# Optimization experiments

Measured on AMD Instinct MI355X. Metric: run time of the kernel, lower is better.

The kernel has to match this reference:

```python
import jax, jax.numpy as jnp
import numpy as np
from jax import lax

C = 128
HEADS = 4
HEAD_DIM = C // HEADS
SCALE = HEAD_DIM ** (-0.5)


def conv2d(x, w, b, pad):
    # x: (B, Cin, H, W), w: (Cout, Cin, kh, kw)
    y = lax.conv_general_dilated(
        x, w, window_strides=(1, 1), padding=[(pad, pad), (pad, pad)],
        dimension_numbers=("NCHW", "OIHW", "NCHW"))
    return y + b[None, :, None, None]


def setup_inputs() -> dict:
    key = jax.random.key(0)
    ks = jax.random.split(key, 16)
    B, H, W = 2, 64, 64
    fan_1x1 = 1.0 / np.sqrt(C)
    fan_3x3a = 1.0 / np.sqrt(1 * 9)
    fan_3x3b = 1.0 / np.sqrt((C // 4) * 9)
    inp = {
        "sr_feat": jax.random.normal(ks[0], (B, C, H, W), jnp.float32),
        "seg_mask": jax.random.uniform(ks[1], (B, 1, H, W), jnp.float32),
        "Wq": jax.random.uniform(ks[2], (C, C, 1, 1), jnp.float32, -fan_1x1, fan_1x1),
        "bq": jnp.zeros((C,), jnp.float32),
        "Wm1": jax.random.uniform(ks[3], (C // 4, 1, 3, 3), jnp.float32, -fan_3x3a, fan_3x3a),
        "bm1": jnp.zeros((C // 4,), jnp.float32),
        "Wm2": jax.random.uniform(ks[4], (C, C // 4, 3, 3), jnp.float32, -fan_3x3b, fan_3x3b),
        "bm2": jnp.zeros((C,), jnp.float32),
        "Wk": jax.random.uniform(ks[5], (C, C, 1, 1), jnp.float32, -fan_1x1, fan_1x1),
        "bk": jnp.zeros((C,), jnp.float32),
        "Wv": jax.random.uniform(ks[6], (C, C, 1, 1), jnp.float32, -fan_1x1, fan_1x1),
        "bv": jnp.zeros((C,), jnp.float32),
        "Wo": jax.random.uniform(ks[7], (C, C, 1, 1), jnp.float32, -fan_1x1, fan_1x1),
        "bo": jnp.zeros((C,), jnp.float32),
    }
    return inp


def reference(sr_feat, seg_mask, Wq, bq, Wm1, bm1, Wm2, bm2, Wk, bk, Wv, bv, Wo, bo):
    B, Cc, H, W = sr_feat.shape
    # mask_embed: conv3x3 -> relu -> conv3x3 (seg_mask already at (H, W))
    mask_feat = conv2d(jax.nn.relu(conv2d(seg_mask, Wm1, bm1, 1)), Wm2, bm2, 1)
    q = conv2d(sr_feat, Wq, bq, 0)
    k = conv2d(mask_feat, Wk, bk, 0)
    v = conv2d(mask_feat, Wv, bv, 0)
    hw = H * W
    # (B, C, HW) -> (B, heads, HW, head_dim)
    def split_heads(t):
        return t.reshape(B, HEADS, HEAD_DIM, hw).transpose(0, 1, 3, 2)
    qh, kh, vh = split_heads(q), split_heads(k), split_heads(v)
    attn = jnp.einsum("bhqd,bhkd->bhqk", qh, kh) * SCALE
    attn = jax.nn.softmax(attn, axis=-1)
    guided = jnp.einsum("bhqk,bhkd->bhqd", attn, vh)  # (B, heads, HW, head_dim)
    guided = guided.transpose(0, 1, 3, 2).reshape(B, Cc, H, W)
    return conv2d(guided, Wo, bo, 0) + sr_feat
```

## Files before the change

kernel.cpp:

```cpp
#include <hip/hip_runtime.h>
#include <hip/hip_bf16.h>

#define HW 4096
#define CC 128
#define SCALE_LOG2E (0.17677669529663687f * 1.4426950408889634f)
#define KSPLIT 8
#define H1PAD 4096

typedef short bf16x8 __attribute__((ext_vector_type(8)));
typedef float f32x4 __attribute__((ext_vector_type(4)));

static __device__ __forceinline__ unsigned short f2bf(float f) {
  unsigned int u = __float_as_uint(f);
  unsigned int r = (u + 0x7fffu + ((u >> 16) & 1u)) >> 16;
  return (unsigned short)r;
}
static __device__ __forceinline__ unsigned int pk2bf(float lo, float hi) {
  return __builtin_amdgcn_perm(__float_as_uint(hi), __float_as_uint(lo),
                               0x07060302u);
}
static __device__ __forceinline__ unsigned int pk2bf_rne(float lo, float hi) {
  return (unsigned int)f2bf(lo) | ((unsigned int)f2bf(hi) << 16);
}
static __device__ __forceinline__ f32x4 mfma16(bf16x8 a, bf16x8 b, f32x4 c) {
  return __builtin_amdgcn_mfma_f32_16x16x32_bf16(a, b, c, 0, 0, 0);
}

__global__ __launch_bounds__(256) void wcast_kernel(
    const float* __restrict__ Wq, const float* __restrict__ Wk,
    const float* __restrict__ Wv, const float* __restrict__ Wo,
    unsigned short* __restrict__ wbf) {
  int i = blockIdx.x * 256 + threadIdx.x;
  int which = i >> 14, j = i & 16383;
  const float* src = which == 0 ? Wq : which == 1 ? Wk : which == 2 ? Wv : Wo;
  float v = src[j];
  if (which == 0) v *= SCALE_LOG2E;
  wbf[i] = f2bf(v);
}

__global__ __launch_bounds__(256) void wcast2_kernel(
    const float* __restrict__ Wm2, unsigned short* __restrict__ wm2t) {
  int i = blockIdx.x * 256 + threadIdx.x;
  int tap = i >> 12;
  int rem = i & 4095;
  int co = rem >> 5, ci = rem & 31;
  wm2t[i] = f2bf(Wm2[co * 288 + ci * 9 + tap]);
}

__global__ __launch_bounds__(256) void conv1_relu_kernel(
    const float* __restrict__ seg, const float* __restrict__ Wm1,
    const float* __restrict__ bm1, unsigned short* __restrict__ h1p) {
  __shared__ float wls[288];
  const int t = threadIdx.x;
  for (int j = t; j < 288; j += 256) wls[j] = Wm1[j];
  const int idx = blockIdx.x * 256 + t;
  const int b = idx >> 12, p = idx & 4095;
  const int x = p & 63, y = p >> 6;
  const float* sb = seg + b * HW;
  float pix[9];
#pragma unroll
  for (int tap = 0; tap < 9; ++tap) {
    int dy = tap / 3 - 1, dx = tap % 3 - 1;
    int xx = x + dx, yy = y + dy;
    bool valid = ((unsigned)xx < 64u) & ((unsigned)yy < 64u);
    pix[tap] = valid ? sb[yy * 64 + xx] : 0.f;
  }
  __syncthreads();
  unsigned int pk[16];
#pragma unroll
  for (int cg = 0; cg < 16; ++cg) {
    float s0 = bm1[2 * cg], s1 = bm1[2 * cg + 1];
#pragma unroll
    for (int tap = 0; tap < 9; ++tap) {
      s0 += wls[(2 * cg) * 9 + tap] * pix[tap];
      s1 += wls[(2 * cg + 1) * 9 + tap] * pix[tap];
    }
    pk[cg] = pk2bf_rne(fmaxf(s0, 0.f), fmaxf(s1, 0.f));
  }
  unsigned short* dst = h1p + (size_t)idx * 32;
#pragma unroll
  for (int g = 0; g < 4; ++g) *(uint4*)(dst + g * 8) = *(uint4*)&pk[g * 4];
}

__global__ __launch_bounds__(256) void conv2_mfma(
    const unsigned short* __restrict__ h1p, const unsigned short* __restrict__ wm2t,
    const float* __restrict__ bm2, unsigned short* __restrict__ mfT) {
  const int b   = blockIdx.y;
  const int px0 = blockIdx.x * 32;
  const int t   = threadIdx.x;
  const int w = t >> 6, lane = t & 63, col = lane & 15, quad = lane >> 4;

  bf16x8 afrag[9][2];
#pragma unroll
  for (int tap = 0; tap < 9; ++tap) {
    const unsigned short* wb =
        wm2t + ((size_t)tap * 128 + w * 32 + col) * 32 + quad * 8;
    afrag[tap][0] = *(const bf16x8*)wb;
    afrag[tap][1] = *(const bf16x8*)(wb + 16 * 32);
  }

  const unsigned short* xb = h1p + (size_t)b * HW * 32;
  f32x4 acc[2][2] = {};
  const bf16x8 zf = {0, 0, 0, 0, 0, 0, 0, 0};

  const int px[2] = {px0 + col, px0 + 16 + col};
  const int xx[2] = {px[0] & 63, px[1] & 63};
  const int yy[2] = {px[0] >> 6, px[1] >> 6};

#pragma unroll
  for (int tap = 0; tap < 9; ++tap) {
    const int dy = tap / 3 - 1, dx = tap % 3 - 1;
    const int shift = dy * 64 + dx;
#pragma unroll
    for (int pt = 0; pt < 2; ++pt) {
      bool valid = ((unsigned)(xx[pt] + dx) < 64u) & ((unsigned)(yy[pt] + dy) < 64u);
      bf16x8 bf = *(const bf16x8*)(xb + (size_t)(px[pt] + shift) * 32 + quad * 8);
      bf = valid ? bf : zf;
      acc[0][pt] = mfma16(afrag[tap][0], bf, acc[0][pt]);
      acc[1][pt] = mfma16(afrag[tap][1], bf, acc[1][pt]);
    }
  }

#pragma unroll
  for (int ct = 0; ct < 2; ++ct) {
    float4 bb = *(const float4*)(bm2 + w * 32 + ct * 16 + quad * 4);
#pragma unroll
    for (int pt = 0; pt < 2; ++pt) {
      int co = w * 32 + ct * 16 + quad * 4;
      uint2 pk = {pk2bf_rne(acc[ct][pt][0] + bb.x, acc[ct][pt][1] + bb.y),
                  pk2bf_rne(acc[ct][pt][2] + bb.z, acc[ct][pt][3] + bb.w)};
      *(uint2*)(mfT + ((size_t)b * HW + px[pt]) * CC + co) = pk;
    }
  }
}

__global__ __launch_bounds__(256) void conv_q_mfma(
    const float* __restrict__ in, const unsigned short* __restrict__ wq,
    const float* __restrict__ bq, unsigned short* __restrict__ qt) {
  const int b   = blockIdx.y;
  const int px0 = blockIdx.x * 32;
  const int t   = threadIdx.x;
  const int w = t >> 6, lane = t & 63, col = lane & 15, quad = lane >> 4;

  __shared__ unsigned short xT[32][136];
  for (int r = 0; r < 16; ++r) {
    int idx = r * 256 + t;
    int ci = idx >> 5, px = idx & 31;
    xT[px][ci] = f2bf(in[((size_t)b * CC + ci) * HW + px0 + px]);
  }
  __syncthreads();

  f32x4 acc[2][2] = {};
  const unsigned short* wbase = wq + (size_t)(w * 32 + col) * CC + quad * 8;
#pragma unroll
  for (int ks = 0; ks < 4; ++ks) {
    bf16x8 a0 = *(const bf16x8*)(wbase + ks * 32);
    bf16x8 a1 = *(const bf16x8*)(wbase + 16 * CC + ks * 32);
    bf16x8 b0 = *(const bf16x8*)&xT[col][ks * 32 + quad * 8];
    bf16x8 b1 = *(const bf16x8*)&xT[16 + col][ks * 32 + quad * 8];
    acc[0][0] = mfma16(a0, b0, acc[0][0]);
    acc[0][1] = mfma16(a0, b1, acc[0][1]);
    acc[1][0] = mfma16(a1, b0, acc[1][0]);
    acc[1][1] = mfma16(a1, b1, acc[1][1]);
  }
  const int bh = b * 4 + w;
#pragma unroll
  for (int ct = 0; ct < 2; ++ct) {
    float4 bb = *(const float4*)(bq + w * 32 + ct * 16 + quad * 4);
#pragma unroll
    for (int pt = 0; pt < 2; ++pt) {
      float r0 = acc[ct][pt][0] + bb.x * SCALE_LOG2E;
      float r1 = acc[ct][pt][1] + bb.y * SCALE_LOG2E;
      float r2 = acc[ct][pt][2] + bb.z * SCALE_LOG2E;
      float r3 = acc[ct][pt][3] + bb.w * SCALE_LOG2E;
      uint2 pk = {pk2bf_rne(r0, r1), pk2bf_rne(r2, r3)};
      *(uint2*)(qt + ((size_t)bh * HW + px0 + pt * 16 + col) * 32 +
                ct * 16 + quad * 4) = pk;
    }
  }
}

__global__ __launch_bounds__(256) void conv_kv_mfma(
    const unsigned short* __restrict__ mfT, const unsigned short* __restrict__ wk,
    const unsigned short* __restrict__ wv, const float* __restrict__ bk,
    const float* __restrict__ bv, unsigned short* __restrict__ kt,
    unsigned short* __restrict__ vt) {
  const int b   = blockIdx.y;
  const int px0 = blockIdx.x * 32;
  const int t   = threadIdx.x;
  const int w = t >> 6, lane = t & 63, col = lane & 15, quad = lane >> 4;

  f32x4 ak[2][2] = {}, av[2][2] = {};
  const unsigned short* wkb = wk + (size_t)(w * 32 + col) * CC + quad * 8;
  const unsigned short* wvb = wv + (size_t)(w * 32 + col) * CC + quad * 8;
  const unsigned short* xb0 = mfT + ((size_t)b * HW + px0 + col) * CC + quad * 8;
  const unsigned short* xb1 = xb0 + (size_t)16 * CC;
#pragma unroll
  for (int ks = 0; ks < 4; ++ks) {
    bf16x8 ka0 = *(const bf16x8*)(wkb + ks * 32);
    bf16x8 ka1 = *(const bf16x8*)(wkb + 16 * CC + ks * 32);
    bf16x8 va0 = *(const bf16x8*)(wvb + ks * 32);
    bf16x8 va1 = *(const bf16x8*)(wvb + 16 * CC + ks * 32);
    bf16x8 b0 = *(const bf16x8*)(xb0 + ks * 32);
    bf16x8 b1 = *(const bf16x8*)(xb1 + ks * 32);
    ak[0][0] = mfma16(ka0, b0, ak[0][0]);
    ak[0][1] = mfma16(ka0, b1, ak[0][1]);
    ak[1][0] = mfma16(ka1, b0, ak[1][0]);
    ak[1][1] = mfma16(ka1, b1, ak[1][1]);
    av[0][0] = mfma16(va0, b0, av[0][0]);
    av[0][1] = mfma16(va0, b1, av[0][1]);
    av[1][0] = mfma16(va1, b0, av[1][0]);
    av[1][1] = mfma16(va1, b1, av[1][1]);
  }
  const int bh = b * 4 + w;
  const int chunk = blockIdx.x;
#pragma unroll
  for (int ct = 0; ct < 2; ++ct) {
    float4 bbk = *(const float4*)(bk + w * 32 + ct * 16 + quad * 4);
    float4 bbv = *(const float4*)(bv + w * 32 + ct * 16 + quad * 4);
#pragma unroll
    for (int pt = 0; pt < 2; ++pt) {
      int key = pt * 16 + col;
      float k0 = ak[ct][pt][0] + bbk.x, k1 = ak[ct][pt][1] + bbk.y;
      float k2 = ak[ct][pt][2] + bbk.z, k3 = ak[ct][pt][3] + bbk.w;
      uint2 pkk = {pk2bf_rne(k0, k1), pk2bf_rne(k2, k3)};
      *(uint2*)(kt + ((size_t)bh * HW + px0 + key) * 32 + ct * 16 + quad * 4) = pkk;
      unsigned short* vdst =
          vt + (((size_t)bh * 128 + chunk) * 32 + ct * 16 + quad * 4) * 32 + key;
      vdst[0]  = f2bf(av[ct][pt][0] + bbv.x);
      vdst[32] = f2bf(av[ct][pt][1] + bbv.y);
      vdst[64] = f2bf(av[ct][pt][2] + bbv.z);
      vdst[96] = f2bf(av[ct][pt][3] + bbv.w);
    }
  }
}

__global__ __launch_bounds__(256, 4) void attn_mfma_kernel(
    const unsigned short* __restrict__ qt, const unsigned short* __restrict__ ktg,
    const unsigned short* __restrict__ vt, unsigned short* __restrict__ opart,
    float* __restrict__ lpart) {
  const int bh   = blockIdx.y;
  const int s    = blockIdx.z;
  const int t    = threadIdx.x;
  const int wave = t >> 6;
  const int lane = t & 63;
  const int col  = lane & 15;
  const int quad = lane >> 4;
  const int q0w  = blockIdx.x * 256 + wave * 64;

  const unsigned short* Qb = qt  + (size_t)bh * HW * 32;
  const unsigned short* Kb = ktg + (size_t)bh * HW * 32;
  const unsigned short* Vc = vt  + (size_t)bh * 128 * 1024;

  __shared__ unsigned short Pt[4][4][16][40];

  bf16x8 qf[4];
#pragma unroll
  for (int qt_i = 0; qt_i < 4; ++qt_i)
    qf[qt_i] = *(const bf16x8*)(Qb + (size_t)(q0w + qt_i * 16 + col) * 32 + quad * 8);

  float lacc[4] = {0.f, 0.f, 0.f, 0.f};
  f32x4 o[4][2] = {};
  const f32x4 zero = {0.f, 0.f, 0.f, 0.f};

  const unsigned short* kp1 = Kb + (size_t)(s * 16) * 1024 + col * 32 + quad * 8;
  const unsigned short* kp2 = kp1 + 512;
  const unsigned short* vp1 = Vc + (size_t)(s * 16) * 1024 + col * 32 + quad * 8;
  const unsigned short* vp2 = vp1 + 512;

  for (int c = 0; c < 16; ++c) {
    bf16x8 kf1 = *(const bf16x8*)(kp1 + c * 1024);
    bf16x8 kf2 = *(const bf16x8*)(kp2 + c * 1024);
    bf16x8 vf1 = *(const bf16x8*)(vp1 + c * 1024);
    bf16x8 vf2 = *(const bf16x8*)(vp2 + c * 1024);
#pragma unroll
    for (int qt_i = 0; qt_i < 4; ++qt_i) {
      f32x4 s1 = mfma16(kf1, qf[qt_i], zero);
      f32x4 s2 = mfma16(kf2, qf[qt_i], zero);
      float p0 = __builtin_amdgcn_exp2f(s1[0]);
      float p1 = __builtin_amdgcn_exp2f(s1[1]);
      float p2 = __builtin_amdgcn_exp2f(s1[2]);
      float p3 = __builtin_amdgcn_exp2f(s1[3]);
      float p4 = __builtin_amdgcn_exp2f(s2[0]);
      float p5 = __builtin_amdgcn_exp2f(s2[1]);
      float p6 = __builtin_amdgcn_exp2f(s2[2]);
      float p7 = __builtin_amdgcn_exp2f(s2[3]);
      lacc[qt_i] += ((p0 + p1) + (p2 + p3)) + ((p4 + p5) + (p6 + p7));

      uint2 w1 = {pk2bf(p0, p1), pk2bf(p2, p3)};
      uint2 w2 = {pk2bf(p4, p5), pk2bf(p6, p7)};
      *(uint2*)&Pt[wave][qt_i][col][quad * 4]      = w1;
      *(uint2*)&Pt[wave][qt_i][col][16 + quad * 4] = w2;
      bf16x8 pf = *(const bf16x8*)&Pt[wave][qt_i][col][quad * 8];

      o[qt_i][0] = mfma16(vf1, pf, o[qt_i][0]);
      o[qt_i][1] = mfma16(vf2, pf, o[qt_i][1]);
    }
  }

#pragma unroll
  for (int qt_i = 0; qt_i < 4; ++qt_i) {
    float l = lacc[qt_i];
    l += __shfl_xor(l, 16);
    l += __shfl_xor(l, 32);
    int qq = q0w + qt_i * 16 + col;
    size_t base = ((size_t)(s * 8 + bh) * HW + qq) * 32;
    uint2 w1 = {pk2bf_rne(o[qt_i][0][0], o[qt_i][0][1]),
                pk2bf_rne(o[qt_i][0][2], o[qt_i][0][3])};
    uint2 w2 = {pk2bf_rne(o[qt_i][1][0], o[qt_i][1][1]),
                pk2bf_rne(o[qt_i][1][2], o[qt_i][1][3])};
    *(uint2*)(opart + base + quad * 4)      = w1;
    *(uint2*)(opart + base + 16 + quad * 4) = w2;
    if (quad == 0) lpart[(size_t)(s * 8 + bh) * HW + qq] = l;
  }
}

__global__ __launch_bounds__(256) void attn_combine_kernel(
    const unsigned short* __restrict__ opart, const float* __restrict__ lpart,
    unsigned short* __restrict__ gdT) {
  const int bh = blockIdx.y;
  const int q  = blockIdx.x * 256 + threadIdx.x;
  const int b  = bh >> 2;
  const int c0 = (bh & 3) * 32;

  float lsum = 0.f;
#pragma unroll
  for (int s = 0; s < KSPLIT; ++s) lsum += lpart[(size_t)(s * 8 + bh) * HW + q];
  float inv = 1.f / lsum;

  float acc[32];
#pragma unroll
  for (int j = 0; j < 32; ++j) acc[j] = 0.f;
#pragma unroll
  for (int s = 0; s < KSPLIT; ++s) {
    const unsigned short* src = opart + ((size_t)(s * 8 + bh) * HW + q) * 32;
#pragma unroll
    for (int g = 0; g < 4; ++g) {
      uint4 raw = *(const uint4*)(src + g * 8);
      const unsigned int* u = (const unsigned int*)&raw;
#pragma unroll
      for (int h = 0; h < 4; ++h) {
        acc[g * 8 + 2 * h]     += __uint_as_float(u[h] << 16);
        acc[g * 8 + 2 * h + 1] += __uint_as_float(u[h] & 0xffff0000u);
      }
    }
  }
  unsigned short* dst = gdT + ((size_t)b * HW + q) * CC + c0;
  unsigned int pk[16];
#pragma unroll
  for (int j = 0; j < 16; ++j)
    pk[j] = pk2bf_rne(acc[2 * j] * inv, acc[2 * j + 1] * inv);
#pragma unroll
  for (int g = 0; g < 4; ++g) *(uint4*)(dst + g * 8) = *(uint4*)&pk[g * 4];
}

__global__ __launch_bounds__(256) void convo_mfma(
    const unsigned short* __restrict__ gdT, const unsigned short* __restrict__ wo,
    const float* __restrict__ bo, const float* __restrict__ sr,
    float* __restrict__ out) {
  const int b   = blockIdx.y;
  const int px0 = blockIdx.x * 64;
  const int t   = threadIdx.x;
  const int w = t >> 6, lane = t & 63, col = lane & 15, quad = lane >> 4;

  f32x4 acc[2][4] = {};
  const unsigned short* wbase = wo + (size_t)(w * 32 + col) * CC + quad * 8;
  const unsigned short* xbase = gdT + ((size_t)b * HW + px0 + col) * CC + quad * 8;
#pragma unroll
  for (int ks = 0; ks < 4; ++ks) {
    bf16x8 a0 = *(const bf16x8*)(wbase + ks * 32);
    bf16x8 a1 = *(const bf16x8*)(wbase + 16 * CC + ks * 32);
#pragma unroll
    for (int pt = 0; pt < 4; ++pt) {
      bf16x8 bfr = *(const bf16x8*)(xbase + (size_t)pt * 16 * CC + ks * 32);
      acc[0][pt] = mfma16(a0, bfr, acc[0][pt]);
      acc[1][pt] = mfma16(a1, bfr, acc[1][pt]);
    }
  }
#pragma unroll
  for (int ct = 0; ct < 2; ++ct) {
    float4 bb = *(const float4*)(bo + w * 32 + ct * 16 + quad * 4);
    float bias[4] = {bb.x, bb.y, bb.z, bb.w};
#pragma unroll
    for (int pt = 0; pt < 4; ++pt) {
      int px = px0 + pt * 16 + col;
      int co = w * 32 + ct * 16 + quad * 4;
      const float* rb = sr + ((size_t)b * CC + co) * HW + px;
      float* ob = out + ((size_t)b * CC + co) * HW + px;
#pragma unroll
      for (int r = 0; r < 4; ++r)
        ob[(size_t)r * HW] = acc[ct][pt][r] + bias[r] + rb[(size_t)r * HW];
    }
  }
}

extern "C" void kernel_launch(void* const* d_in, const int* in_sizes, int n_in,
                              void* d_out, int out_size, void* d_ws, size_t ws_size,
                              hipStream_t stream) {
  const float* sr  = (const float*)d_in[0];
  const float* seg = (const float*)d_in[1];
  const float* Wq  = (const float*)d_in[2];
  const float* bq  = (const float*)d_in[3];
  const float* Wm1 = (const float*)d_in[4];
  const float* bm1 = (const float*)d_in[5];
  const float* Wm2 = (const float*)d_in[6];
  const float* bm2 = (const float*)d_in[7];
  const float* Wk  = (const float*)d_in[8];
  const float* bk  = (const float*)d_in[9];
  const float* Wv  = (const float*)d_in[10];
  const float* bv  = (const float*)d_in[11];
  const float* Wo  = (const float*)d_in[12];
  const float* bo  = (const float*)d_in[13];
  float* out = (float*)d_out;

  unsigned short* h1T = (unsigned short*)d_ws;
  unsigned short* h1p = h1T + H1PAD;
  unsigned short* mfT = h1T + H1PAD + 262144 + H1PAD;
  unsigned short* qt  = mfT + 1048576;
  unsigned short* kt  = qt + 1048576;
  unsigned short* vt  = kt + 1048576;
  unsigned short* gdT = vt + 1048576;
  unsigned short* wbf = gdT + 1048576;
  unsigned short* wm2t = wbf + 65536;
  unsigned short* opart = wm2t + 36864;
  float* lpart = (float*)(opart + (size_t)KSPLIT * 8 * HW * 32);

  const unsigned short* wq = wbf;
  const unsigned short* wk = wbf + 16384;
  const unsigned short* wv = wbf + 32768;
  const unsigned short* wo = wbf + 49152;

  wcast_kernel<<<256, 256, 0, stream>>>(Wq, Wk, Wv, Wo, wbf);
  wcast2_kernel<<<144, 256, 0, stream>>>(Wm2, wm2t);
  conv1_relu_kernel<<<32, 256, 0, stream>>>(seg, Wm1, bm1, h1p);
  conv2_mfma<<<dim3(128, 2), 256, 0, stream>>>(h1p, wm2t, bm2, mfT);
  conv_q_mfma<<<dim3(128, 2), 256, 0, stream>>>(sr, wq, bq, qt);
  conv_kv_mfma<<<dim3(128, 2), 256, 0, stream>>>(mfT, wk, wv, bk, bv, kt, vt);
  attn_mfma_kernel<<<dim3(16, 8, KSPLIT), 256, 0, stream>>>(qt, kt, vt, opart, lpart);
  attn_combine_kernel<<<dim3(16, 8), 256, 0, stream>>>(opart, lpart, gdT);
  convo_mfma<<<dim3(64, 2), 256, 0, stream>>>(gdT, wo, bo, sr, out);
}
```

Measured before the change: 142.6 us.

## Fuse prep, conv2+QKV, and combine+out-proj kernels; prefetch K/V in attention

Merges the three weight-cast and conv1 kernels into one prep kernel with block-range dispatch. Fuses conv2 with the Q/K/V 1x1 projections through shared memory, and fuses the split-K combine with the output projection, so the mfT and gdT intermediates never go to global memory. In the attention loop, the next chunk's K/V fragments are loaded one iteration ahead. This cuts launch count and global traffic, at the cost of more registers and shared memory per block. The prefetch also reads one chunk past the last iteration.

```diff
diff --git a/kernel.cpp b/kernel.cpp
--- a/kernel.cpp
+++ b/kernel.cpp
@@ -26,204 +26,171 @@
   return __builtin_amdgcn_mfma_f32_16x16x32_bf16(a, b, c, 0, 0, 0);
 }
 
-__global__ __launch_bounds__(256) void wcast_kernel(
+__global__ __launch_bounds__(256) void prep_kernel(
     const float* __restrict__ Wq, const float* __restrict__ Wk,
     const float* __restrict__ Wv, const float* __restrict__ Wo,
-    unsigned short* __restrict__ wbf) {
-  int i = blockIdx.x * 256 + threadIdx.x;
-  int which = i >> 14, j = i & 16383;
-  const float* src = which == 0 ? Wq : which == 1 ? Wk : which == 2 ? Wv : Wo;
-  float v = src[j];
-  if (which == 0) v *= SCALE_LOG2E;
-  wbf[i] = f2bf(v);
-}
-
-__global__ __launch_bounds__(256) void wcast2_kernel(
-    const float* __restrict__ Wm2, unsigned short* __restrict__ wm2t) {
-  int i = blockIdx.x * 256 + threadIdx.x;
-  int tap = i >> 12;
-  int rem = i & 4095;
-  int co = rem >> 5, ci = rem & 31;
-  wm2t[i] = f2bf(Wm2[co * 288 + ci * 9 + tap]);
-}
-
-__global__ __launch_bounds__(256) void conv1_relu_kernel(
-    const float* __restrict__ seg, const float* __restrict__ Wm1,
-    const float* __restrict__ bm1, unsigned short* __restrict__ h1p) {
+    const float* __restrict__ Wm2, const float* __restrict__ seg,
+    const float* __restrict__ Wm1, const float* __restrict__ bm1,
+    unsigned short* __restrict__ wbf, unsigned short* __restrict__ wm2t,
+    unsigned short* __restrict__ h1p) {
   __shared__ float wls[288];
+  const int blk = blockIdx.x;
   const int t = threadIdx.x;
-  for (int j = t; j < 288; j += 256) wls[j] = Wm1[j];
-  const int idx = blockIdx.x * 256 + t;
-  const int b = idx >> 12, p = idx & 4095;
-  const int x = p & 63, y = p >> 6;
-  const float* sb = seg + b * HW;
-  float pix[9];
-#pragma unroll
-  for (int tap = 0; tap < 9; ++tap) {
-    int dy = tap / 3 - 1, dx = tap % 3 - 1;
-    int xx = x + dx, yy = y + dy;
-    bool valid = ((unsigned)xx < 64u) & ((unsigned)yy < 64u);
-    pix[tap] = valid ? sb[yy * 64 + xx] : 0.f;
-  }
-  __syncthreads();
-  unsigned int pk[16];
-#pragma unroll
-  for (int cg = 0; cg < 16; ++cg) {
-    float s0 = bm1[2 * cg], s1 = bm1[2 * cg + 1];
+  if (blk < 256) {
+    int i = blk * 256 + t;
+    int which = i >> 14, j = i & 16383;
+    const float* src = which == 0 ? Wq : which == 1 ? Wk : which == 2 ? Wv : Wo;
+    float v = src[j];
+    if (which == 0) v *= SCALE_LOG2E;
+    wbf[i] = f2bf(v);
+  } else if (blk < 400) {
+    int i = (blk - 256) * 256 + t;
+    int tap = i >> 12;
+    int rem = i & 4095;
+    int co = rem >> 5, ci = rem & 31;
+    wm2t[i] = f2bf(Wm2[co * 288 + ci * 9 + tap]);
+  } else {
+    for (int j = t; j < 288; j += 256) wls[j] = Wm1[j];
+    const int idx = (blk - 400) * 256 + t;
+    const int b = idx >> 12, p = idx & 4095;
+    const int x = p & 63, y = p >> 6;
+    const float* sb = seg + b * HW;
+    float pix[9];
 #pragma unroll
     for (int tap = 0; tap < 9; ++tap) {
-      s0 += wls[(2 * cg) * 9 + tap] * pix[tap];
-      s1 += wls[(2 * cg + 1) * 9 + tap] * pix[tap];
-    }
-    pk[cg] = pk2bf_rne(fmaxf(s0, 0.f), fmaxf(s1, 0.f));
-  }
-  unsigned short* dst = h1p + (size_t)idx * 32;
-#pragma unroll
-  for (int g = 0; g < 4; ++g) *(uint4*)(dst + g * 8) = *(uint4*)&pk[g * 4];
-}
-
-__global__ __launch_bounds__(256) void conv2_mfma(
-    const unsigned short* __restrict__ h1p, const unsigned short* __restrict__ wm2t,
-    const float* __restrict__ bm2, unsigned short* __restrict__ mfT) {
-  const int b   = blockIdx.y;
-  const int px0 = blockIdx.x * 32;
-  const int t   = threadIdx.x;
-  const int w = t >> 6, lane = t & 63, col = lane & 15, quad = lane >> 4;
-
-  bf16x8 afrag[9][2];
-#pragma unroll
-  for (int tap = 0; tap < 9; ++tap) {
-    const unsigned short* wb =
-        wm2t + ((size_t)tap * 128 + w * 32 + col) * 32 + quad * 8;
-    afrag[tap][0] = *(const bf16x8*)wb;
-    afrag[tap][1] = *(const bf16x8*)(wb + 16 * 32);
-  }
-
-  const unsigned short* xb = h1p + (size_t)b * HW * 32;
-  f32x4 acc[2][2] = {};
-  const bf16x8 zf = {0, 0, 0, 0, 0, 0, 0, 0};
-
-  const int px[2] = {px0 + col, px0 + 16 + col};
-  const int xx[2] = {px[0] & 63, px[1] & 63};
-  const int yy[2] = {px[0] >> 6, px[1] >> 6};
-
-#pragma unroll
-  for (int tap = 0; tap < 9; ++tap) {
-    const int dy = tap / 3 - 1, dx = tap % 3 - 1;
-    const int shift = dy * 64 + dx;
-#pragma unroll
-    for (int pt = 0; pt < 2; ++pt) {
-      bool valid = ((unsigned)(xx[pt] + dx) < 64u) & ((unsigned)(yy[pt] + dy) < 64u);
-      bf16x8 bf = *(const bf16x8*)(xb + (size_t)(px[pt] + shift) * 32 + quad * 8);
-      bf = valid ? bf : zf;
-      acc[0][pt] = mfma16(afrag[tap][0], bf, acc[0][pt]);
-      acc[1][pt] = mfma16(afrag[tap][1], bf, acc[1][pt]);
-    }
-  }
-
-#pragma unroll
-  for (int ct = 0; ct < 2; ++ct) {
-    float4 bb = *(const float4*)(bm2 + w * 32 + ct * 16 + quad * 4);
-#pragma unroll
-    for (int pt = 0; pt < 2; ++pt) {
-      int co = w * 32 + ct * 16 + quad * 4;
-      uint2 pk = {pk2bf_rne(acc[ct][pt][0] + bb.x, acc[ct][pt][1] + bb.y),
-                  pk2bf_rne(acc[ct][pt][2] + bb.z, acc[ct][pt][3] + bb.w)};
-      *(uint2*)(mfT + ((size_t)b * HW + px[pt]) * CC + co) = pk;
-    }
-  }
-}
-
-__global__ __launch_bounds__(256) void conv_q_mfma(
-    const float* __restrict__ in, const unsigned short* __restrict__ wq,
-    const float* __restrict__ bq, unsigned short* __restrict__ qt) {
-  const int b   = blockIdx.y;
-  const int px0 = blockIdx.x * 32;
-  const int t   = threadIdx.x;
-  const int w = t >> 6, lane = t & 63, col = lane & 15, quad = lane >> 4;
-
-  __shared__ unsigned short xT[32][136];
-  for (int r = 0; r < 16; ++r) {
-    int idx = r * 256 + t;
-    int ci = idx >> 5, px = idx & 31;
-    xT[px][ci] = f2bf(in[((size_t)b * CC + ci) * HW + px0 + px]);
-  }
-  __syncthreads();
-
-  f32x4 acc[2][2] = {};
-  const unsigned short* wbase = wq + (size_t)(w * 32 + col) * CC + quad * 8;
-#pragma unroll
-  for (int ks = 0; ks < 4; ++ks) {
-    bf16x8 a0 = *(const bf16x8*)(wbase + ks * 32);
-    bf16x8 a1 = *(const bf16x8*)(wbase + 16 * CC + ks * 32);
-    bf16x8 b0 = *(const bf16x8*)&xT[col][ks * 32 + quad * 8];
-    bf16x8 b1 = *(const bf16x8*)&xT[16 + col][ks * 32 + quad * 8];
-    acc[0][0] = mfma16(a0, b0, acc[0][0]);
-    acc[0][1] = mfma16(a0, b1, acc[0][1]);
-    acc[1][0] = mfma16(a1, b0, acc[1][0]);
-    acc[1][1] = mfma16(a1, b1, acc[1][1]);
-  }
-  const int bh = b * 4 + w;
-#pragma unroll
-  for (int ct = 0; ct < 2; ++ct) {
-    float4 bb = *(const float4*)(bq + w * 32 + ct * 16 + quad * 4);
-#pragma unroll
-    for (int pt = 0; pt < 2; ++pt) {
-      float r0 = acc[ct][pt][0] + bb.x * SCALE_LOG2E;
-      float r1 = acc[ct][pt][1] + bb.y * SCALE_LOG2E;
-      float r2 = acc[ct][pt][2] + bb.z * SCALE_LOG2E;
-      float r3 = acc[ct][pt][3] + bb.w * SCALE_LOG2E;
-      uint2 pk = {pk2bf_rne(r0, r1), pk2bf_rne(r2, r3)};
-      *(uint2*)(qt + ((size_t)bh * HW + px0 + pt * 16 + col) * 32 +
-                ct * 16 + quad * 4) = pk;
-    }
-  }
-}
-
-__global__ __launch_bounds__(256) void conv_kv_mfma(
-    const unsigned short* __restrict__ mfT, const unsigned short* __restrict__ wk,
-    const unsigned short* __restrict__ wv, const float* __restrict__ bk,
-    const float* __restrict__ bv, unsigned short* __restrict__ kt,
+      int dy = tap / 3 - 1, dx = tap % 3 - 1;
+      int xx = x + dx, yy = y + dy;
+      bool valid = ((unsigned)xx < 64u) & ((unsigned)yy < 64u);
+      pix[tap] = valid ? sb[yy * 64 + xx] : 0.f;
+    }
+    __syncthreads();
+    unsigned int pk[16];
+#pragma unroll
+    for (int cg = 0; cg < 16; ++cg) {
+      float s0 = bm1[2 * cg], s1 = bm1[2 * cg + 1];
+#pragma unroll
+      for (int tap = 0; tap < 9; ++tap) {
+        s0 += wls[(2 * cg) * 9 + tap] * pix[tap];
+        s1 += wls[(2 * cg + 1) * 9 + tap] * pix[tap];
+      }
+      pk[cg] = pk2bf_rne(fmaxf(s0, 0.f), fmaxf(s1, 0.f));
+    }
+    unsigned short* dst = h1p + (size_t)idx * 32;
+#pragma unroll
+    for (int g = 0; g < 4; ++g) *(uint4*)(dst + g * 8) = *(uint4*)&pk[g * 4];
+  }
+}
+
+__global__ __launch_bounds__(256) void conv2qkv_mfma(
+    const float* __restrict__ sr, const unsigned short* __restrict__ h1p,
+    const unsigned short* __restrict__ wm2t, const float* __restrict__ bm2,
+    const unsigned short* __restrict__ wq, const float* __restrict__ bq,
+    const unsigned short* __restrict__ wk, const float* __restrict__ bk,
+    const unsigned short* __restrict__ wv, const float* __restrict__ bv,
+    unsigned short* __restrict__ qt, unsigned short* __restrict__ kt,
     unsigned short* __restrict__ vt) {
   const int b   = blockIdx.y;
   const int px0 = blockIdx.x * 32;
   const int t   = threadIdx.x;
   const int w = t >> 6, lane = t & 63, col = lane & 15, quad = lane >> 4;
 
-  f32x4 ak[2][2] = {}, av[2][2] = {};
+  __shared__ unsigned short mT[32][136];
+  __shared__ unsigned short xT[32][136];
+
+  for (int r = 0; r < 16; ++r) {
+    int idx = r * 256 + t;
+    int ci = idx >> 5, px = idx & 31;
+    xT[px][ci] = f2bf(sr[((size_t)b * CC + ci) * HW + px0 + px]);
+  }
+
+  {
+    bf16x8 afrag[9][2];
+#pragma unroll
+    for (int tap = 0; tap < 9; ++tap) {
+      const unsigned short* wb =
+          wm2t + ((size_t)tap * 128 + w * 32 + col) * 32 + quad * 8;
+      afrag[tap][0] = *(const bf16x8*)wb;
+      afrag[tap][1] = *(const bf16x8*)(wb + 16 * 32);
+    }
+    const unsigned short* xb = h1p + (size_t)b * HW * 32;
+    f32x4 acc[2][2] = {};
+    const bf16x8 zf = {0, 0, 0, 0, 0, 0, 0, 0};
+    const int px[2] = {px0 + col, px0 + 16 + col};
+    const int xx[2] = {px[0] & 63, px[1] & 63};
+    const int yy[2] = {px[0] >> 6, px[1] >> 6};
+#pragma unroll
+    for (int tap = 0; tap < 9; ++tap) {
+      const int dy = tap / 3 - 1, dx = tap % 3 - 1;
+      const int shift = dy * 64 + dx;
+#pragma unroll
+      for (int pt = 0; pt < 2; ++pt) {
+        bool valid =
+            ((unsigned)(xx[pt] + dx) < 64u) & ((unsigned)(yy[pt] + dy) < 64u);
+        bf16x8 bf = *(const bf16x8*)(xb + (size_t)(px[pt] + shift) * 32 + quad * 8);
+        bf = valid ? bf : zf;
+        acc[0][pt] = mfma16(afrag[tap][0], bf, acc[0][pt]);
+        acc[1][pt] = mfma16(afrag[tap][1], bf, acc[1][pt]);
+      }
+    }
+#pragma unroll
+    for (int ct = 0; ct < 2; ++ct) {
+      float4 bb = *(const float4*)(bm2 + w * 32 + ct * 16 + quad * 4);
+#pragma unroll
+      for (int pt = 0; pt < 2; ++pt) {
+        uint2 pk = {pk2bf_rne(acc[ct][pt][0] + bb.x, acc[ct][pt][1] + bb.y),
+                    pk2bf_rne(acc[ct][pt][2] + bb.z, acc[ct][pt][3] + bb.w)};
+        *(uint2*)&mT[pt * 16 + col][w * 32 + ct * 16 + quad * 4] = pk;
+      }
+    }
+  }
+  __syncthreads();
+
+  f32x4 aq[2][2] = {}, ak[2][2] = {}, av[2][2] = {};
+  const unsigned short* wqb = wq + (size_t)(w * 32 + col) * CC + quad * 8;
   const unsigned short* wkb = wk + (size_t)(w * 32 + col) * CC + quad * 8;
   const unsigned short* wvb = wv + (size_t)(w * 32 + col) * CC + quad * 8;
-  const unsigned short* xb0 = mfT + ((size_t)b * HW + px0 + col) * CC + quad * 8;
-  const unsigned short* xb1 = xb0 + (size_t)16 * CC;
 #pragma unroll
   for (int ks = 0; ks < 4; ++ks) {
+    bf16x8 qa0 = *(const bf16x8*)(wqb + ks * 32);
+    bf16x8 qa1 = *(const bf16x8*)(wqb + 16 * CC + ks * 32);
     bf16x8 ka0 = *(const bf16x8*)(wkb + ks * 32);
     bf16x8 ka1 = *(const bf16x8*)(wkb + 16 * CC + ks * 32);
     bf16x8 va0 = *(const bf16x8*)(wvb + ks * 32);
     bf16x8 va1 = *(const bf16x8*)(wvb + 16 * CC + ks * 32);
-    bf16x8 b0 = *(const bf16x8*)(xb0 + ks * 32);
-    bf16x8 b1 = *(const bf16x8*)(xb1 + ks * 32);
-    ak[0][0] = mfma16(ka0, b0, ak[0][0]);
-    ak[0][1] = mfma16(ka0, b1, ak[0][1]);
-    ak[1][0] = mfma16(ka1, b0, ak[1][0]);
-    ak[1][1] = mfma16(ka1, b1, ak[1][1]);
-    av[0][0] = mfma16(va0, b0, av[0][0]);
-    av[0][1] = mfma16(va0, b1, av[0][1]);
-    av[1][0] = mfma16(va1, b0, av[1][0]);
-    av[1][1] = mfma16(va1, b1, av[1][1]);
+    bf16x8 bx0 = *(const bf16x8*)&xT[col][ks * 32 + quad * 8];
+    bf16x8 bx1 = *(const bf16x8*)&xT[16 + col][ks * 32 + quad * 8];
+    bf16x8 bm0 = *(const bf16x8*)&mT[col][ks * 32 + quad * 8];
+    bf16x8 bm1f = *(const bf16x8*)&mT[16 + col][ks * 32 + quad * 8];
+    aq[0][0] = mfma16(qa0, bx0, aq[0][0]);
+    aq[0][1] = mfma16(qa0, bx1, aq[0][1]);
+    aq[1][0] = mfma16(qa1, bx0, aq[1][0]);
+    aq[1][1] = mfma16(qa1, bx1, aq[1][1]);
+    ak[0][0] = mfma16(ka0, bm0, ak[0][0]);
+    ak[0][1] = mfma16(ka0, bm1f, ak[0][1]);
+    ak[1][0] = mfma16(ka1, bm0, ak[1][0]);
+    ak[1][1] = mfma16(ka1, bm1f, ak[1][1]);
+    av[0][0] = mfma16(va0, bm0, av[0][0]);
+    av[0][1] = mfma16(va0, bm1f, av[0][1]);
+    av[1][0] = mfma16(va1, bm0, av[1][0]);
+    av[1][1] = mfma16(va1, bm1f, av[1][1]);
   }
   const int bh = b * 4 + w;
   const int chunk = blockIdx.x;
 #pragma unroll
   for (int ct = 0; ct < 2; ++ct) {
+    float4 bbq = *(const float4*)(bq + w * 32 + ct * 16 + quad * 4);
     float4 bbk = *(const float4*)(bk + w * 32 + ct * 16 + quad * 4);
     float4 bbv = *(const float4*)(bv + w * 32 + ct * 16 + quad * 4);
 #pragma unroll
     for (int pt = 0; pt < 2; ++pt) {
       int key = pt * 16 + col;
-      float k0 = ak[ct][pt][0] + bbk.x, k1 = ak[ct][pt][1] + bbk.y;
-      float k2 = ak[ct][pt][2] + bbk.z, k3 = ak[ct][pt][3] + bbk.w;
-      uint2 pkk = {pk2bf_rne(k0, k1), pk2bf_rne(k2, k3)};
+      uint2 pkq = {pk2bf_rne(aq[ct][pt][0] + bbq.x * SCALE_LOG2E,
+                             aq[ct][pt][1] + bbq.y * SCALE_LOG2E),
+                   pk2bf_rne(aq[ct][pt][2] + bbq.z * SCALE_LOG2E,
+                             aq[ct][pt][3] + bbq.w * SCALE_LOG2E)};
+      *(uint2*)(qt + ((size_t)bh * HW + px0 + key) * 32 + ct * 16 + quad * 4) = pkq;
+      uint2 pkk = {pk2bf_rne(ak[ct][pt][0] + bbk.x, ak[ct][pt][1] + bbk.y),
+                   pk2bf_rne(ak[ct][pt][2] + bbk.z, ak[ct][pt][3] + bbk.w)};
       *(uint2*)(kt + ((size_t)bh * HW + px0 + key) * 32 + ct * 16 + quad * 4) = pkk;
       unsigned short* vdst =
           vt + (((size_t)bh * 128 + chunk) * 32 + ct * 16 + quad * 4) * 32 + key;
@@ -268,11 +235,16 @@
   const unsigned short* vp1 = Vc + (size_t)(s * 16) * 1024 + col * 32 + quad * 8;
   const unsigned short* vp2 = vp1 + 512;
 
+  bf16x8 kf1 = *(const bf16x8*)(kp1);
+  bf16x8 kf2 = *(const bf16x8*)(kp2);
+  bf16x8 vf1 = *(const bf16x8*)(vp1);
+  bf16x8 vf2 = *(const bf16x8*)(vp2);
+
   for (int c = 0; c < 16; ++c) {
-    bf16x8 kf1 = *(const bf16x8*)(kp1 + c * 1024);
-    bf16x8 kf2 = *(const bf16x8*)(kp2 + c * 1024);
-    bf16x8 vf1 = *(const bf16x8*)(vp1 + c * 1024);
-    bf16x8 vf2 = *(const bf16x8*)(vp2 + c * 1024);
+    bf16x8 nk1 = *(const bf16x8*)(kp1 + (c + 1) * 1024);
+    bf16x8 nk2 = *(const bf16x8*)(kp2 + (c + 1) * 1024);
+    bf16x8 nv1 = *(const bf16x8*)(vp1 + (c + 1) * 1024);
+    bf16x8 nv2 = *(const bf16x8*)(vp2 + (c + 1) * 1024);
 #pragma unroll
     for (int qt_i = 0; qt_i < 4; ++qt_i) {
       f32x4 s1 = mfma16(kf1, qf[qt_i], zero);
@@ -296,6 +268,7 @@
       o[qt_i][0] = mfma16(vf1, pf, o[qt_i][0]);
       o[qt_i][1] = mfma16(vf2, pf, o[qt_i][1]);
     }
+    kf1 = nk1; kf2 = nk2; vf1 = nv1; vf2 = nv2;
   }
 
 #pragma unroll
@@ -315,81 +288,79 @@
   }
 }
 
-__global__ __launch_bounds__(256) void attn_combine_kernel(
+__global__ __launch_bounds__(256) void combine_convo(
     const unsigned short* __restrict__ opart, const float* __restrict__ lpart,
-    unsigned short* __restrict__ gdT) {
-  const int bh = blockIdx.y;
-  const int q  = blockIdx.x * 256 + threadIdx.x;
-  const int b  = bh >> 2;
-  const int c0 = (bh & 3) * 32;
-
-  float lsum = 0.f;
-#pragma unroll
-  for (int s = 0; s < KSPLIT; ++s) lsum += lpart[(size_t)(s * 8 + bh) * HW + q];
-  float inv = 1.f / lsum;
-
-  float acc[32];
-#pragma unroll
-  for (int j = 0; j < 32; ++j) acc[j] = 0.f;
-#pragma unroll
-  for (int s = 0; s < KSPLIT; ++s) {
-    const unsigned short* src = opart + ((size_t)(s * 8 + bh) * HW + q) * 32;
-#pragma unroll
-    for (int g = 0; g < 4; ++g) {
-      uint4 raw = *(const uint4*)(src + g * 8);
-      const unsigned int* u = (const unsigned int*)&raw;
-#pragma unroll
-      for (int h = 0; h < 4; ++h) {
-        acc[g * 8 + 2 * h]     += __uint_as_float(u[h] << 16);
-        acc[g * 8 + 2 * h + 1] += __uint_as_float(u[h] & 0xffff0000u);
+    const unsigned short* __restrict__ wo, const float* __restrict__ bo,
+    const float* __restrict__ sr, float* __restrict__ out) {
+  const int b   = blockIdx.y;
+  const int px0 = blockIdx.x * 32;
+  const int t   = threadIdx.x;
+
+  __shared__ unsigned short gT[32][136];
+
+  {
+    const int px = t & 31, cs = t >> 5;
+    const int q  = px0 + px;
+    const int bh = b * 4 + (cs >> 1);
+    const int d0 = (cs & 1) * 16;
+    float lsum = 0.f;
+#pragma unroll
+    for (int s = 0; s < KSPLIT; ++s) lsum += lpart[(size_t)(s * 8 + bh) * HW + q];
+    float inv = 1.f / lsum;
+    float acc[16];
+#pragma unroll
+    for (int j = 0; j < 16; ++j) acc[j] = 0.f;
+#pragma unroll
+    for (int s = 0; s < KSPLIT; ++s) {
+      const unsigned short* src =
+          opart + ((size_t)(s * 8 + bh) * HW + q) * 32 + d0;
+#pragma unroll
+      for (int g = 0; g < 2; ++g) {
+        uint4 raw = *(const uint4*)(src + g * 8);
+        const unsigned int* u = (const unsigned int*)&raw;
+#pragma unroll
+        for (int h = 0; h < 4; ++h) {
+          acc[g * 8 + 2 * h]     += __uint_as_float(u[h] << 16);
+          acc[g * 8 + 2 * h + 1] += __uint_as_float(u[h] & 0xffff0000u);
+        }
       }
     }
-  }
-  unsigned short* dst = gdT + ((size_t)b * HW + q) * CC + c0;
-  unsigned int pk[16];
-#pragma unroll
-  for (int j = 0; j < 16; ++j)
-    pk[j] = pk2bf_rne(acc[2 * j] * inv, acc[2 * j + 1] * inv);
-#pragma unroll
-  for (int g = 0; g < 4; ++g) *(uint4*)(dst + g * 8) = *(uint4*)&pk[g * 4];
-}
-
-__global__ __launch_bounds__(256) void convo_mfma(
-    const unsigned short* __restrict__ gdT, const unsigned short* __restrict__ wo,
-    const float* __restrict__ bo, const float* __restrict__ sr,
-    float* __restrict__ out) {
-  const int b   = blockIdx.y;
-  const int px0 = blockIdx.x * 64;
-  const int t   = threadIdx.x;
+    unsigned int pk[8];
+#pragma unroll
+    for (int j = 0; j < 8; ++j)
+      pk[j] = pk2bf_rne(acc[2 * j] * inv, acc[2 * j + 1] * inv);
+    *(uint4*)&gT[px][cs * 16]     = *(uint4*)&pk[0];
+    *(uint4*)&gT[px][cs * 16 + 8] = *(uint4*)&pk[4];
+  }
+  __syncthreads();
+
   const int w = t >> 6, lane = t & 63, col = lane & 15, quad = lane >> 4;
-
-  f32x4 acc[2][4] = {};
+  f32x4 acc2[2][2] = {};
   const unsigned short* wbase = wo + (size_t)(w * 32 + col) * CC + quad * 8;
-  const unsigned short* xbase = gdT + ((size_t)b * HW + px0 + col) * CC + quad * 8;
 #pragma unroll
   for (int ks = 0; ks < 4; ++ks) {
     bf16x8 a0 = *(const bf16x8*)(wbase + ks * 32);
     bf16x8 a1 = *(const bf16x8*)(wbase + 16 * CC + ks * 32);
-#pragma unroll
-    for (int pt = 0; pt < 4; ++pt) {
-      bf16x8 bfr = *(const bf16x8*)(xbase + (size_t)pt * 16 * CC + ks * 32);
-      acc[0][pt] = mfma16(a0, bfr, acc[0][pt]);
-      acc[1][pt] = mfma16(a1, bfr, acc[1][pt]);
-    }
+    bf16x8 b0 = *(const bf16x8*)&gT[col][ks * 32 + quad * 8];
+    bf16x8 b1 = *(const bf16x8*)&gT[16 + col][ks * 32 + quad * 8];
+    acc2[0][0] = mfma16(a0, b0, acc2[0][0]);
+    acc2[0][1] = mfma16(a0, b1, acc2[0][1]);
+    acc2[1][0] = mfma16(a1, b0, acc2[1][0]);
+    acc2[1][1] = mfma16(a1, b1, acc2[1][1]);
   }
 #pragma unroll
   for (int ct = 0; ct < 2; ++ct) {
     float4 bb = *(const float4*)(bo + w * 32 + ct * 16 + quad * 4);
     float bias[4] = {bb.x, bb.y, bb.z, bb.w};
 #pragma unroll
-    for (int pt = 0; pt < 4; ++pt) {
+    for (int pt = 0; pt < 2; ++pt) {
       int px = px0 + pt * 16 + col;
       int co = w * 32 + ct * 16 + quad * 4;
       const float* rb = sr + ((size_t)b * CC + co) * HW + px;
       float* ob = out + ((size_t)b * CC + co) * HW + px;
 #pragma unroll
       for (int r = 0; r < 4; ++r)
-        ob[(size_t)r * HW] = acc[ct][pt][r] + bias[r] + rb[(size_t)r * HW];
+        ob[(size_t)r * HW] = acc2[ct][pt][r] + bias[r] + rb[(size_t)r * HW];
     }
   }
 }
@@ -415,12 +386,10 @@
 
   unsigned short* h1T = (unsigned short*)d_ws;
   unsigned short* h1p = h1T + H1PAD;
-  unsigned short* mfT = h1T + H1PAD + 262144 + H1PAD;
-  unsigned short* qt  = mfT + 1048576;
+  unsigned short* qt  = h1T + H1PAD + 262144 + H1PAD;
   unsigned short* kt  = qt + 1048576;
   unsigned short* vt  = kt + 1048576;
-  unsigned short* gdT = vt + 1048576;
-  unsigned short* wbf = gdT + 1048576;
+  unsigned short* wbf = vt + 1048576;
   unsigned short* wm2t = wbf + 65536;
   unsigned short* opart = wm2t + 36864;
   float* lpart = (float*)(opart + (size_t)KSPLIT * 8 * HW * 32);
@@ -430,13 +399,11 @@
   const unsigned short* wv = wbf + 32768;
   const unsigned short* wo = wbf + 49152;
 
-  wcast_kernel<<<256, 256, 0, stream>>>(Wq, Wk, Wv, Wo, wbf);
-  wcast2_kernel<<<144, 256, 0, stream>>>(Wm2, wm2t);
-  conv1_relu_kernel<<<32, 256, 0, stream>>>(seg, Wm1, bm1, h1p);
-  conv2_mfma<<<dim3(128, 2), 256, 0, stream>>>(h1p, wm2t, bm2, mfT);
-  conv_q_mfma<<<dim3(128, 2), 256, 0, stream>>>(sr, wq, bq, qt);
-  conv_kv_mfma<<<dim3(128, 2), 256, 0, stream>>>(mfT, wk, wv, bk, bv, kt, vt);
-  attn_mfma_kernel<<<dim3(16, 8, KSPLIT), 256, 0, stream>>>(qt, kt, vt, opart, lpart);
-  attn_combine_kernel<<<dim3(16, 8), 256, 0, stream>>>(opart, lpart, gdT);
-  convo_mfma<<<dim3(64, 2), 256, 0, stream>>>(gdT, wo, bo, sr, out);
-}
+  prep_kernel<<<432, 256, 0, stream>>>(Wq, Wk, Wv, Wo, Wm2, seg, Wm1, bm1,
+                                       wbf, wm2t, h1p);
+  conv2qkv_mfma<<<dim3(128, 2), 256, 0, stream>>>(
+      sr, h1p, wm2t, bm2, wq, bq, wk, bk, wv, bv, qt, kt, vt);
+  attn_mfma_kernel<<<dim3(16, 8, KSPLIT), 256, 0, stream>>>(qt, kt, vt, opart,
+                                                            lpart);
+  combine_convo<<<dim3(128, 2), 256, 0, stream>>>(opart, lpart, wo, bo, sr, out);
+}
```

New measurement: 130.6 us, median of 2. 8.4% less time.
